# Performance work log

Measured on AMD Instinct MI355X. Metric: run time of the kernel, lower is better.

## Reference

```python
import jax, jax.numpy as jnp
import numpy as np

B, T, D, H, DH, F, E, TOPK = 4, 1024, 1024, 16, 64, 4096, 8, 2
GATE_TEMP = 0.9
EPS = 1e-5


def _ln(x, g, b):
    m = jnp.mean(x, axis=-1, keepdims=True)
    v = jnp.mean((x - m) ** 2, axis=-1, keepdims=True)
    return (x - m) * jax.lax.rsqrt(v + EPS) * g + b


def setup_inputs() -> dict:
    key = jax.random.key(0)
    ks = jax.random.split(key, 16)
    s = 0.02
    inp = {
        'x': jax.random.normal(ks[0], (B, T, D), jnp.float32),
        'mask': jnp.tril(jnp.ones((1, 1, T, T), jnp.int32)),  # causal
        'ln1_g': jnp.ones((D,), jnp.float32), 'ln1_b': jnp.zeros((D,), jnp.float32),
        'wq': jax.random.normal(ks[1], (D, D), jnp.float32) * s, 'bq': jnp.zeros((D,), jnp.float32),
        'wk': jax.random.normal(ks[2], (D, D), jnp.float32) * s, 'bk': jnp.zeros((D,), jnp.float32),
        'wv': jax.random.normal(ks[3], (D, D), jnp.float32) * s, 'bv': jnp.zeros((D,), jnp.float32),
        'wo': jax.random.normal(ks[4], (D, D), jnp.float32) * s, 'bo': jnp.zeros((D,), jnp.float32),
        'ln2_g': jnp.ones((D,), jnp.float32), 'ln2_b': jnp.zeros((D,), jnp.float32),
        'gate_w': jax.random.normal(ks[5], (D, E), jnp.float32) * s, 'gate_b': jnp.zeros((E,), jnp.float32),
        'we1': jax.random.normal(ks[6], (E, D, F), jnp.float32) * s, 'be1': jnp.zeros((E, F), jnp.float32),
        'we2': jax.random.normal(ks[7], (E, F, D), jnp.float32) * s, 'be2': jnp.zeros((E, D), jnp.float32),
        'pn_g': jnp.ones((D,), jnp.float32), 'pn_b': jnp.zeros((D,), jnp.float32),
    }
    return inp


def reference(x, mask, ln1_g, ln1_b, wq, bq, wk, bk, wv, bv, wo, bo,
              ln2_g, ln2_b, gate_w, gate_b, we1, be1, we2, be2, pn_g, pn_b):
    # ---- attention branch (dropout = identity in eval) ----
    h = _ln(x, ln1_g, ln1_b)
    q = (h @ wq + bq).reshape(B, T, H, DH).transpose(0, 2, 1, 3)  # [B,H,T,DH]
    k = (h @ wk + bk).reshape(B, T, H, DH).transpose(0, 2, 1, 3)
    v = (h @ wv + bv).reshape(B, T, H, DH).transpose(0, 2, 1, 3)
    att = jnp.einsum('bhtd,bhsd->bhts', q, k) / jnp.sqrt(jnp.float32(DH))
    att = jnp.where(mask == 0, jnp.float32(-1e9), att)
    att = jax.nn.softmax(att, axis=-1)
    out = jnp.einsum('bhts,bhsd->bhtd', att, v).transpose(0, 2, 1, 3).reshape(B, T, D)
    x = x + (out @ wo + bo)

    # ---- MoE branch ----
    h = _ln(x, ln2_g, ln2_b)
    gate_logits = (h @ gate_w + gate_b) / GATE_TEMP        # [B,T,E]
    topk_vals, topk_idx = jax.lax.top_k(gate_logits, TOPK)
    keep = jnp.sum(jax.nn.one_hot(topk_idx, E, dtype=bool), axis=-2)  # [B,T,E] bool
    masked = jnp.where(keep, gate_logits, -jnp.inf)
    gate_probs = jax.nn.softmax(masked, axis=-1)            # [B,T,E]
    # dense all-expert FFN (exact GELU, dropout=identity)
    hid = jax.nn.gelu(jnp.einsum('btd,edf->btef', h, we1) + be1, approximate=False)
    expert_out = jnp.einsum('btef,efd->bted', hid, we2) + be2  # [B,T,E,D]
    moe = jnp.sum(gate_probs[..., None] * expert_out, axis=2)
    moe = _ln(moe, pn_g, pn_b)
    return x + moe
```

## Files before the change

### kernel.cpp

```cpp
#include <hip/hip_runtime.h>
#include <hip/hip_bf16.h>
#include <math.h>

#define B_ 4
#define T_ 1024
#define D_ 1024
#define H_ 16
#define DH_ 64
#define F_ 4096
#define E_ 8
#define NTOK 4096
#define EPS_ 1e-5f

typedef float f32x4 __attribute__((ext_vector_type(4)));
typedef __bf16 bf16x8 __attribute__((ext_vector_type(8)));
typedef _Float16 f16x8 __attribute__((ext_vector_type(8)));

__device__ __forceinline__ unsigned short f2bf(float f) {
    unsigned u = __float_as_uint(f);
    u = u + 0x7fffu + ((u >> 16) & 1u);
    return (unsigned short)(u >> 16);
}

__device__ __forceinline__ void splitf(float x, unsigned short& h, unsigned short& l) {
    _Float16 hf = (_Float16)x;
    _Float16 lf = (_Float16)((x - (float)hf) * 2048.0f);
    h = __builtin_bit_cast(unsigned short, hf);
    l = __builtin_bit_cast(unsigned short, lf);
}

__device__ __forceinline__ float erf_fast(float x) {
    float ax = fabsf(x);
    float t = 1.0f / fmaf(0.3275911f, ax, 1.0f);
    float y = t * fmaf(t, fmaf(t, fmaf(t, fmaf(t, 1.061405429f, -1.453152027f),
                  1.421413741f), -0.284496736f), 0.254829592f);
    float r = 1.0f - y * __expf(-ax * ax);
    return copysignf(r, x);
}

__device__ __forceinline__ void gload16(const unsigned short* g, unsigned short* l) {
    __builtin_amdgcn_global_load_lds(
        (const __attribute__((address_space(1))) unsigned int*)g,
        (__attribute__((address_space(3))) unsigned int*)l,
        16, 0, 0);
}

__device__ __forceinline__ void blockreduce2(float& s, float& sq) {
    #pragma unroll
    for (int o = 32; o > 0; o >>= 1) { s += __shfl_xor(s, o); sq += __shfl_xor(sq, o); }
    __shared__ float ls[4], lq[4];
    int w = threadIdx.x >> 6;
    if ((threadIdx.x & 63) == 0) { ls[w] = s; lq[w] = sq; }
    __syncthreads();
    s = ls[0] + ls[1] + ls[2] + ls[3];
    sq = lq[0] + lq[1] + lq[2] + lq[3];
}

__global__ void k_zero(int* __restrict__ cnt) {
    if (threadIdx.x < E_) cnt[threadIdx.x] = 0;
}

__global__ void k_tconv(const float* __restrict__ in, unsigned short* __restrict__ out,
                        int R, int C) {
    __shared__ float tile[32][33];
    int e = blockIdx.z;
    const float* ine = in + (size_t)e * R * C;
    unsigned short* oute = out + (size_t)e * R * C;
    int tx = threadIdx.x & 31, ty = threadIdx.x >> 5;
    int c0 = blockIdx.x * 32, r0 = blockIdx.y * 32;
    #pragma unroll
    for (int j = 0; j < 32; j += 8)
        tile[ty + j][tx] = ine[(size_t)(r0 + ty + j) * C + c0 + tx];
    __syncthreads();
    #pragma unroll
    for (int j = 0; j < 32; j += 8)
        oute[(size_t)(c0 + ty + j) * R + r0 + tx] = f2bf(tile[tx][ty + j]);
}

__global__ void k_tconv_split(const float* __restrict__ w0, const float* __restrict__ w1,
        const float* __restrict__ w2, const float* __restrict__ w3,
        unsigned short* __restrict__ ohi, unsigned short* __restrict__ olo) {
    __shared__ float tile[32][33];
    int z = blockIdx.z;
    const float* in = (z == 0) ? w0 : ((z == 1) ? w1 : ((z == 2) ? w2 : w3));
    unsigned short* oh = ohi + (size_t)z * D_ * D_;
    unsigned short* ol = olo + (size_t)z * D_ * D_;
    int tx = threadIdx.x & 31, ty = threadIdx.x >> 5;
    int c0 = blockIdx.x * 32, r0 = blockIdx.y * 32;
    #pragma unroll
    for (int j = 0; j < 32; j += 8)
        tile[ty + j][tx] = in[(size_t)(r0 + ty + j) * D_ + c0 + tx];
    __syncthreads();
    #pragma unroll
    for (int j = 0; j < 32; j += 8) {
        unsigned short h, l;
        splitf(tile[tx][ty + j], h, l);
        size_t o = (size_t)(c0 + ty + j) * D_ + r0 + tx;
        oh[o] = h; ol[o] = l;
    }
}

__global__ void k_ln1(const float* __restrict__ x, const float* __restrict__ g,
                      const float* __restrict__ b, unsigned short* __restrict__ hh,
                      unsigned short* __restrict__ hl) {
    int row = blockIdx.x, t = threadIdx.x;
    f32x4 v = *(const f32x4*)(x + (size_t)row * D_ + t * 4);
    float s = v.x + v.y + v.z + v.w;
    float sq = v.x * v.x + v.y * v.y + v.z * v.z + v.w * v.w;
    blockreduce2(s, sq);
    float mean = s * (1.0f / D_);
    float var = sq * (1.0f / D_) - mean * mean;
    float inv = rsqrtf(var + EPS_);
    f32x4 gv = *(const f32x4*)(g + t * 4);
    f32x4 bv = *(const f32x4*)(b + t * 4);
    ushort4 oh, ol;
    float o0 = (v.x - mean) * inv * gv.x + bv.x;
    float o1 = (v.y - mean) * inv * gv.y + bv.y;
    float o2 = (v.z - mean) * inv * gv.z + bv.z;
    float o3 = (v.w - mean) * inv * gv.w + bv.w;
    splitf(o0, oh.x, ol.x); splitf(o1, oh.y, ol.y);
    splitf(o2, oh.z, ol.z); splitf(o3, oh.w, ol.w);
    *(ushort4*)(hh + (size_t)row * D_ + t * 4) = oh;
    *(ushort4*)(hl + (size_t)row * D_ + t * 4) = ol;
}

#define LDK2 40
__device__ __forceinline__ void mfma_split(const unsigned short* __restrict__ Ah,
        const unsigned short* __restrict__ Al, int strideA, int m0,
        const unsigned short* __restrict__ Bh, const unsigned short* __restrict__ Bl,
        int strideB, int n0, int K, f32x4 acc1[4][4], f32x4 acc2[4][4]) {
    __shared__ unsigned short AsH[128 * LDK2];
    __shared__ unsigned short AsL[128 * LDK2];
    __shared__ unsigned short BsH[128 * LDK2];
    __shared__ unsigned short BsL[128 * LDK2];
    int t = threadIdx.x;
    int lane = t & 63, w = t >> 6;
    int wm = (w >> 1) * 64, wn = (w & 1) * 64;
    int r = t >> 1, kc = (t & 1) * 16;
    const unsigned short* pAh = Ah + (size_t)(m0 + r) * strideA + kc;
    const unsigned short* pAl = Al + (size_t)(m0 + r) * strideA + kc;
    const unsigned short* pBh = Bh + (size_t)(n0 + r) * strideB + kc;
    const unsigned short* pBl = Bl + (size_t)(n0 + r) * strideB + kc;
    int c15 = lane & 15, fk = (lane >> 4) * 8;
    unsigned short* wAh = &AsH[r * LDK2 + kc];
    unsigned short* wAl = &AsL[r * LDK2 + kc];
    unsigned short* wBh = &BsH[r * LDK2 + kc];
    unsigned short* wBl = &BsL[r * LDK2 + kc];
    uint4 ah0 = *(const uint4*)(pAh);
    uint4 ah1 = *(const uint4*)(pAh + 8);
    uint4 al0 = *(const uint4*)(pAl);
    uint4 al1 = *(const uint4*)(pAl + 8);
    uint4 bh0 = *(const uint4*)(pBh);
    uint4 bh1 = *(const uint4*)(pBh + 8);
    uint4 bl0 = *(const uint4*)(pBl);
    uint4 bl1 = *(const uint4*)(pBl + 8);
    for (int k0 = 0; k0 < K; k0 += 32) {
        __syncthreads();
        *(uint4*)(wAh) = ah0; *(uint4*)(wAh + 8) = ah1;
        *(uint4*)(wAl) = al0; *(uint4*)(wAl + 8) = al1;
        *(uint4*)(wBh) = bh0; *(uint4*)(wBh + 8) = bh1;
        *(uint4*)(wBl) = bl0; *(uint4*)(wBl + 8) = bl1;
        __syncthreads();
        if (k0 + 32 < K) {
            ah0 = *(const uint4*)(pAh + k0 + 32);
            ah1 = *(const uint4*)(pAh + k0 + 40);
            al0 = *(const uint4*)(pAl + k0 + 32);
            al1 = *(const uint4*)(pAl + k0 + 40);
            bh0 = *(const uint4*)(pBh + k0 + 32);
            bh1 = *(const uint4*)(pBh + k0 + 40);
            bl0 = *(const uint4*)(pBl + k0 + 32);
            bl1 = *(const uint4*)(pBl + k0 + 40);
        }
        f16x8 bfh[4], bfl[4];
        #pragma unroll
        for (int i = 0; i < 4; i++) {
            bfh[i] = *(const f16x8*)(&BsH[(wn + c15 + i * 16) * LDK2 + fk]);
            bfl[i] = *(const f16x8*)(&BsL[(wn + c15 + i * 16) * LDK2 + fk]);
        }
        #pragma unroll
        for (int mi = 0; mi < 4; mi++) {
            f16x8 afh = *(const f16x8*)(&AsH[(wm + c15 + mi * 16) * LDK2 + fk]);
            f16x8 afl = *(const f16x8*)(&AsL[(wm + c15 + mi * 16) * LDK2 + fk]);
            #pragma unroll
            for (int ni = 0; ni < 4; ni++) {
                acc1[mi][ni] = __builtin_amdgcn_mfma_f32_16x16x32_f16(afh, bfh[ni], acc1[mi][ni], 0, 0, 0);
                acc2[mi][ni] = __builtin_amdgcn_mfma_f32_16x16x32_f16(afh, bfl[ni], acc2[mi][ni], 0, 0, 0);
                acc2[mi][ni] = __builtin_amdgcn_mfma_f32_16x16x32_f16(afl, bfh[ni], acc2[mi][ni], 0, 0, 0);
            }
        }
    }
}

__global__ __launch_bounds__(256, 2) void k_qkv_split(
        const unsigned short* __restrict__ h1h, const unsigned short* __restrict__ h1l,
        const unsigned short* __restrict__ wth, const unsigned short* __restrict__ wtl,
        const float* __restrict__ bq, const float* __restrict__ bk, const float* __restrict__ bv,
        unsigned short* __restrict__ Qh, unsigned short* __restrict__ Ql,
        unsigned short* __restrict__ Kh, unsigned short* __restrict__ Kl,
        unsigned short* __restrict__ Vh, unsigned short* __restrict__ Vl) {
    int which = blockIdx.z;
    const unsigned short* Bh = wth + (size_t)which * D_ * D_;
    const unsigned short* Bl = wtl + (size_t)which * D_ * D_;
    const float* bias = (which == 0) ? bq : ((which == 1) ? bk : bv);
    unsigned short* Oh = (which == 0) ? Qh : ((which == 1) ? Kh : Vh);
    unsigned short* Ol = (which == 0) ? Ql : ((which == 1) ? Kl : Vl);
    f32x4 a1[4][4], a2[4][4];
    #pragma unroll
    for (int i = 0; i < 4; i++)
        #pragma unroll
        for (int j = 0; j < 4; j++) {
            a1[i][j].x = 0.f; a1[i][j].y = 0.f; a1[i][j].z = 0.f; a1[i][j].w = 0.f;
            a2[i][j].x = 0.f; a2[i][j].y = 0.f; a2[i][j].z = 0.f; a2[i][j].w = 0.f;
        }
    int m0 = blockIdx.y * 128, n0 = blockIdx.x * 128;
    mfma_split(h1h, h1l, D_, m0, Bh, Bl, D_, n0, D_, a1, a2);
    int lane = threadIdx.x & 63, w = threadIdx.x >> 6;
    int wm = (w >> 1) * 64, wn = (w & 1) * 64;
    int c15 = lane & 15, quad = lane >> 4;
    #pragma unroll
    for (int mi = 0; mi < 4; mi++) {
        #pragma unroll
        for (int rr = 0; rr < 4; rr++) {
            int row = m0 + wm + mi * 16 + quad * 4 + rr;
            int bidx = row >> 10, tt = row & 1023;
            #pragma unroll
            for (int ni = 0; ni < 4; ni++) {
                int col = n0 + wn + ni * 16 + c15;
                float vv = a1[mi][ni][rr] + a2[mi][ni][rr] * (1.0f / 2048.0f) + bias[col];
                unsigned short hs, ls;
                splitf(vv, hs, ls);
                size_t idx = (((size_t)bidx * H_ + (col >> 6)) * T_ + tt) * DH_ + (col & 63);
                Oh[idx] = hs; Ol[idx] = ls;
            }
        }
    }
}

__global__ __launch_bounds__(256, 2) void k_proj_split(
        const unsigned short* __restrict__ ah, const unsigned short* __restrict__ al,
        const unsigned short* __restrict__ wh, const unsigned short* __restrict__ wl,
        float* __restrict__ xp) {
    int ks = blockIdx.z;
    f32x4 a1[4][4], a2[4][4];
    #pragma unroll
    for (int i = 0; i < 4; i++)
        #pragma unroll
        for (int j = 0; j < 4; j++) {
            a1[i][j].x = 0.f; a1[i][j].y = 0.f; a1[i][j].z = 0.f; a1[i][j].w = 0.f;
            a2[i][j].x = 0.f; a2[i][j].y = 0.f; a2[i][j].z = 0.f; a2[i][j].w = 0.f;
        }
    int m0 = blockIdx.y * 128, n0 = blockIdx.x * 128;
    mfma_split(ah + ks * 512, al + ks * 512, D_, m0,
               wh + ks * 512, wl + ks * 512, D_, n0, 512, a1, a2);
    float* dst = xp + (size_t)ks * NTOK * D_;
    int lane = threadIdx.x & 63, w = threadIdx.x >> 6;
    int wm = (w >> 1) * 64, wn = (w & 1) * 64;
    int c15 = lane & 15, quad = lane >> 4;
    #pragma unroll
    for (int mi = 0; mi < 4; mi++) {
        #pragma unroll
        for (int rr = 0; rr < 4; rr++) {
            int row = m0 + wm + mi * 16 + quad * 4 + rr;
            #pragma unroll
            for (int ni = 0; ni < 4; ni++) {
                int col = n0 + wn + ni * 16 + c15;
                dst[(size_t)row * D_ + col] = a1[mi][ni][rr] + a2[mi][ni][rr] * (1.0f / 2048.0f);
            }
        }
    }
}

#define NSLOT 40
__device__ __forceinline__ int slot_base(int qt) {
    const int base[16] = {0,1,2,3,4,6,8,10,12,15,18,21,24,28,32,36};
    return base[qt];
}
__device__ __forceinline__ int swzb(int r, int cb) {
    return r * 128 + (cb ^ ((r & 7) << 4));
}
__global__ __launch_bounds__(256, 2) void k_attn1(
        const unsigned short* __restrict__ Qh, const unsigned short* __restrict__ Ql,
        const unsigned short* __restrict__ Kh, const unsigned short* __restrict__ Kl,
        const unsigned short* __restrict__ Vh, const unsigned short* __restrict__ Vl,
        float* __restrict__ opart, float* __restrict__ mlpart) {
    __shared__ unsigned short QsH[64 * 64], QsL[64 * 64];
    __shared__ unsigned short KsH[64 * 64], KsL[64 * 64];
    __shared__ unsigned short VtH[64 * 64], VtL[64 * 64];
    __shared__ unsigned short PsH[64 * 64], PsL[64 * 64];
    int sp = blockIdx.x, qt = blockIdx.y, bh = blockIdx.z;
    int lim = (qt + 1) * 64;
    int s0 = sp * 256;
    if (s0 >= lim) return;
    int ntile = min(4, (lim - s0) >> 6);
    int t = threadIdx.x;
    int lane = t & 63, w = t >> 6;
    int c15 = lane & 15, quad = lane >> 4;
    size_t bho = (size_t)bh * T_ * DH_;
    {
        int q = t >> 2, cb = (t & 3) * 32;
        const unsigned short* sh = Qh + bho + (size_t)(qt * 64 + q) * DH_ + (cb >> 1);
        const unsigned short* sl = Ql + bho + (size_t)(qt * 64 + q) * DH_ + (cb >> 1);
        uint4 h0 = *(const uint4*)(sh);
        uint4 h1 = *(const uint4*)(sh + 8);
        uint4 l0 = *(const uint4*)(sl);
        uint4 l1 = *(const uint4*)(sl + 8);
        *(uint4*)((char*)QsH + swzb(q, cb))      = h0;
        *(uint4*)((char*)QsH + swzb(q, cb + 16)) = h1;
        *(uint4*)((char*)QsL + swzb(q, cb))      = l0;
        *(uint4*)((char*)QsL + swzb(q, cb + 16)) = l1;
    }
    f32x4 o1[4], o2[4];
    #pragma unroll
    for (int i = 0; i < 4; i++) {
        o1[i].x = 0.f; o1[i].y = 0.f; o1[i].z = 0.f; o1[i].w = 0.f;
        o2[i].x = 0.f; o2[i].y = 0.f; o2[i].z = 0.f; o2[i].w = 0.f;
    }
    float m[4] = {-1e30f, -1e30f, -1e30f, -1e30f};
    float l[4] = {0.f, 0.f, 0.f, 0.f};
    int qglob0 = qt * 64 + w * 16 + quad * 4;
    for (int kt = 0; kt < ntile; kt++) {
        int kbase = s0 + kt * 64;
        __syncthreads();
        {
            int r = t >> 2, cb = (t & 3) * 32;
            const unsigned short* sh = Kh + bho + (size_t)(kbase + r) * DH_ + (cb >> 1);
            const unsigned short* sl = Kl + bho + (size_t)(kbase + r) * DH_ + (cb >> 1);
            uint4 h0 = *(const uint4*)(sh);
            uint4 h1 = *(const uint4*)(sh + 8);
            uint4 l0 = *(const uint4*)(sl);
            uint4 l1 = *(const uint4*)(sl + 8);
            *(uint4*)((char*)KsH + swzb(r, cb))      = h0;
            *(uint4*)((char*)KsH + swzb(r, cb + 16)) = h1;
            *(uint4*)((char*)KsL + swzb(r, cb))      = l0;
            *(uint4*)((char*)KsL + swzb(r, cb + 16)) = l1;
        }
        {
            int k = t & 63, d0 = (t >> 6) * 16;
            const unsigned short* vh = Vh + bho + (size_t)(kbase + k) * DH_ + d0;
            const unsigned short* vl = Vl + bho + (size_t)(kbase + k) * DH_ + d0;
            unsigned short hv[16], lv[16];
            *(uint4*)(hv) = *(const uint4*)(vh);
            *(uint4*)(hv + 8) = *(const uint4*)(vh + 8);
            *(uint4*)(lv) = *(const uint4*)(vl);
            *(uint4*)(lv + 8) = *(const uint4*)(vl + 8);
            #pragma unroll
            for (int i = 0; i < 16; i++) {
                int d = d0 + i;
                *(unsigned short*)((char*)VtH + swzb(d, k * 2)) = hv[i];
                *(unsigned short*)((char*)VtL + swzb(d, k * 2)) = lv[i];
            }
        }
        __syncthreads();
        f32x4 s1[4], s2[4];
        #pragma unroll
        for (int i = 0; i < 4; i++) {
            s1[i].x = 0.f; s1[i].y = 0.f; s1[i].z = 0.f; s1[i].w = 0.f;
            s2[i].x = 0.f; s2[i].y = 0.f; s2[i].z = 0.f; s2[i].w = 0.f;
        }
        #pragma unroll
        for (int kk = 0; kk < 2; kk++) {
            int cb = kk * 64 + quad * 16;
            f16x8 ah = *(const f16x8*)((char*)QsH + swzb(w * 16 + c15, cb));
            f16x8 al = *(const f16x8*)((char*)QsL + swzb(w * 16 + c15, cb));
            #pragma unroll
            for (int ni = 0; ni < 4; ni++) {
                f16x8 bh16 = *(const f16x8*)((char*)KsH + swzb(ni * 16 + c15, cb));
                f16x8 bl16 = *(const f16x8*)((char*)KsL + swzb(ni * 16 + c15, cb));
                s1[ni] = __builtin_amdgcn_mfma_f32_16x16x32_f16(ah, bh16, s1[ni], 0, 0, 0);
                s2[ni] = __builtin_amdgcn_mfma_f32_16x16x32_f16(ah, bl16, s2[ni], 0, 0, 0);
                s2[ni] = __builtin_amdgcn_mfma_f32_16x16x32_f16(al, bh16, s2[ni], 0, 0, 0);
            }
        }
        f32x4 p[4];
        #pragma unroll
        for (int ni = 0; ni < 4; ni++)
            p[ni] = s1[ni] * 0.125f + s2[ni] * 6.103515625e-5f;
        #pragma unroll
        for (int ni = 0; ni < 4; ni++) {
            int kglob = kbase + c15 + 16 * ni;
            #pragma unroll
            for (int r = 0; r < 4; r++)
                p[ni][r] = (kglob <= qglob0 + r) ? p[ni][r] : -1e30f;
        }
        float alpha[4];
        #pragma unroll
        for (int r = 0; r < 4; r++) {
            float rm = fmaxf(fmaxf(p[0][r], p[1][r]), fmaxf(p[2][r], p[3][r]));
            rm = fmaxf(rm, __shfl_xor(rm, 1));
            rm = fmaxf(rm, __shfl_xor(rm, 2));
            rm = fmaxf(rm, __shfl_xor(rm, 4));
            rm = fmaxf(rm, __shfl_xor(rm, 8));
            float mnew = fmaxf(m[r], rm);
            alpha[r] = __expf(m[r] - mnew);
            m[r] = mnew;
            float rs = 0.f;
            #pragma unroll
            for (int ni = 0; ni < 4; ni++) {
                float pv = (p[ni][r] > -1e29f) ? __expf(p[ni][r] - mnew) : 0.f;
                p[ni][r] = pv;
                rs += pv;
            }
            rs += __shfl_xor(rs, 1);
            rs += __shfl_xor(rs, 2);
            rs += __shfl_xor(rs, 4);
            rs += __shfl_xor(rs, 8);
            l[r] = l[r] * alpha[r] + rs;
        }
        #pragma unroll
        for (int ni = 0; ni < 4; ni++) {
            o1[ni].x *= alpha[0]; o1[ni].y *= alpha[1]; o1[ni].z *= alpha[2]; o1[ni].w *= alpha[3];
            o2[ni].x *= alpha[0]; o2[ni].y *= alpha[1]; o2[ni].z *= alpha[2]; o2[ni].w *= alpha[3];
        }
        #pragma unroll
        for (int ni = 0; ni < 4; ni++) {
            int cbyte = (c15 + 16 * ni) * 2;
            #pragma unroll
            for (int r = 0; r < 4; r++) {
                unsigned short hs, ls;
                splitf(p[ni][r], hs, ls);
                int row = w * 16 + quad * 4 + r;
                *(unsigned short*)((char*)PsH + swzb(row, cbyte)) = hs;
                *(unsigned short*)((char*)PsL + swzb(row, cbyte)) = ls;
            }
        }
        __syncthreads();
        #pragma unroll
        for (int kk = 0; kk < 2; kk++) {
            int cb = kk * 64 + quad * 16;
            f16x8 ph = *(const f16x8*)((char*)PsH + swzb(w * 16 + c15, cb));
            f16x8 pl = *(const f16x8*)((char*)PsL + swzb(w * 16 + c15, cb));
            #pragma unroll
            for (int ni = 0; ni < 4; ni++) {
                f16x8 vh16 = *(const f16x8*)((char*)VtH + swzb(ni * 16 + c15, cb));
                f16x8 vl16 = *(const f16x8*)((char*)VtL + swzb(ni * 16 + c15, cb));
                o1[ni] = __builtin_amdgcn_mfma_f32_16x16x32_f16(ph, vh16, o1[ni], 0, 0, 0);
                o2[ni] = __builtin_amdgcn_mfma_f32_16x16x32_f16(ph, vl16, o2[ni], 0, 0, 0);
                o2[ni] = __builtin_amdgcn_mfma_f32_16x16x32_f16(pl, vh16, o2[ni], 0, 0, 0);
            }
        }
    }
    int slot = bh * NSLOT + slot_base(qt) + sp;
    float* dst = opart + (size_t)slot * 64 * 64;
    #pragma unroll
    for (int ni = 0; ni < 4; ni++) {
        #pragma unroll
        for (int r = 0; r < 4; r++) {
            float val = o1[ni][r] + o2[ni][r] * (1.0f / 2048.0f);
            dst[(size_t)(w * 16 + quad * 4 + r) * 64 + c15 + 16 * ni] = val;
        }
    }
    if (c15 == 0) {
        #pragma unroll
        for (int r = 0; r < 4; r++) {
            int row = w * 16 + quad * 4 + r;
            mlpart[slot * 128 + row * 2 + 0] = m[r];
            mlpart[slot * 128 + row * 2 + 1] = l[r];
        }
    }
}

__global__ void k_attn2(const float* __restrict__ opart, const float* __restrict__ mlpart,
                        unsigned short* __restrict__ atth, unsigned short* __restrict__ attl) {
    int qt = blockIdx.x, bh = blockIdx.y;
    int b = bh >> 4, h = bh & 15;
    int nsp = (qt >> 2) + 1;
    int slot0 = bh * NSLOT + slot_base(qt);
    int tid = threadIdx.x;
    int q = tid >> 2, d0 = (tid & 3) * 16;
    float ms[4], ls[4];
    float mx = -1e30f;
    for (int s = 0; s < nsp; s++) {
        ms[s] = mlpart[(slot0 + s) * 128 + q * 2 + 0];
        ls[s] = mlpart[(slot0 + s) * 128 + q * 2 + 1];
        mx = fmaxf(mx, ms[s]);
    }
    float den = 0.f;
    f32x4 num[4];
    #pragma unroll
    for (int i = 0; i < 4; i++) { num[i].x = 0.f; num[i].y = 0.f; num[i].z = 0.f; num[i].w = 0.f; }
    for (int s = 0; s < nsp; s++) {
        float sc = __expf(ms[s] - mx);
        den += ls[s] * sc;
        const float* src = opart + ((size_t)(slot0 + s) * 64 + q) * 64 + d0;
        #pragma unroll
        for (int i = 0; i < 4; i++) num[i] += sc * *(const f32x4*)(src + i * 4);
    }
    float inv = 1.0f / den;
    size_t base = ((size_t)(b * T_ + qt * 64 + q)) * D_ + h * DH_ + d0;
    #pragma unroll
    for (int i = 0; i < 4; i++) {
        f32x4 v = num[i] * inv;
        ushort4 hh, ll;
        splitf(v.x, hh.x, ll.x); splitf(v.y, hh.y, ll.y);
        splitf(v.z, hh.z, ll.z); splitf(v.w, hh.w, ll.w);
        *(ushort4*)(atth + base + i * 4) = hh;
        *(ushort4*)(attl + base + i * 4) = ll;
    }
}

__global__ void k_ln2_gate(const float* __restrict__ xp, const float* __restrict__ bo,
        const float* __restrict__ xin, float* __restrict__ x2,
        const float* __restrict__ g, const float* __restrict__ bb,
        const float* __restrict__ gw, const float* __restrict__ gb,
        unsigned short* __restrict__ h2, int* __restrict__ cnt, int* __restrict__ lst,
        int* __restrict__ te, int* __restrict__ ts, float* __restrict__ tp) {
    int row = blockIdx.x, t = threadIdx.x;
    f32x4 v = *(const f32x4*)(xp + (size_t)row * D_ + t * 4)
            + *(const f32x4*)(xp + (size_t)NTOK * D_ + (size_t)row * D_ + t * 4)
            + *(const f32x4*)(bo + t * 4)
            + *(const f32x4*)(xin + (size_t)row * D_ + t * 4);
    *(f32x4*)(x2 + (size_t)row * D_ + t * 4) = v;
    float s = v.x + v.y + v.z + v.w;
    float sq = v.x * v.x + v.y * v.y + v.z * v.z + v.w * v.w;
    blockreduce2(s, sq);
    float mean = s * (1.0f / D_), var = sq * (1.0f / D_) - mean * mean;
    float inv = rsqrtf(var + EPS_);
    f32x4 gv = *(const f32x4*)(g + t * 4);
    f32x4 bv = *(const f32x4*)(bb + t * 4);
    float hv[4];
    #pragma unroll
    for (int i = 0; i < 4; i++) hv[i] = (v[i] - mean) * inv * gv[i] + bv[i];
    ushort4 hb;
    hb.x = f2bf(hv[0]); hb.y = f2bf(hv[1]); hb.z = f2bf(hv[2]); hb.w = f2bf(hv[3]);
    *(ushort4*)(&h2[(size_t)row * D_ + t * 4]) = hb;
    float lg[8];
    #pragma unroll
    for (int e2 = 0; e2 < 8; e2++) lg[e2] = 0.f;
    #pragma unroll
    for (int i = 0; i < 4; i++) {
        const float* gr = gw + (size_t)(t * 4 + i) * E_;
        f32x4 g0 = *(const f32x4*)(gr);
        f32x4 g1 = *(const f32x4*)(gr + 4);
        lg[0] = fmaf(hv[i], g0.x, lg[0]); lg[1] = fmaf(hv[i], g0.y, lg[1]);
        lg[2] = fmaf(hv[i], g0.z, lg[2]); lg[3] = fmaf(hv[i], g0.w, lg[3]);
        lg[4] = fmaf(hv[i], g1.x, lg[4]); lg[5] = fmaf(hv[i], g1.y, lg[5]);
        lg[6] = fmaf(hv[i], g1.z, lg[6]); lg[7] = fmaf(hv[i], g1.w, lg[7]);
    }
    #pragma unroll
    for (int o = 32; o > 0; o >>= 1) {
        #pragma unroll
        for (int e2 = 0; e2 < 8; e2++) lg[e2] += __shfl_xor(lg[e2], o);
    }
    __shared__ float lred[4][8];
    int w = t >> 6;
    if ((t & 63) == 0) {
        #pragma unroll
        for (int e2 = 0; e2 < 8; e2++) lred[w][e2] = lg[e2];
    }
    __syncthreads();
    if (t == 0) {
        float L[8];
        #pragma unroll
        for (int e2 = 0; e2 < 8; e2++)
            L[e2] = (lred[0][e2] + lred[1][e2] + lred[2][e2] + lred[3][e2] + gb[e2]) / 0.9f;
        int e0 = 0, e1 = -1; float v0 = L[0], v1 = -3e38f;
        #pragma unroll
        for (int e2 = 1; e2 < 8; e2++) {
            float xv = L[e2];
            if (xv > v0)      { v1 = v0; e1 = e0; v0 = xv; e0 = e2; }
            else if (xv > v1) { v1 = xv; e1 = e2; }
        }
        float ex = __expf(v1 - v0);
        float denom = 1.0f + ex;
        float p0 = 1.0f / denom, p1 = ex / denom;
        int s0 = atomicAdd(&cnt[e0], 1);
        int s1 = atomicAdd(&cnt[e1], 1);
        lst[e0 * NTOK + s0] = row;
        lst[e1 * NTOK + s1] = row;
        te[row * 2 + 0] = e0; te[row * 2 + 1] = e1;
        ts[row * 2 + 0] = s0; ts[row * 2 + 1] = s1;
        tp[row * 2 + 0] = p0; tp[row * 2 + 1] = p1;
    }
}

__global__ void k_offs(const int* __restrict__ cnt, int* __restrict__ offs) {
    if (threadIdx.x == 0 && blockIdx.x == 0) {
        int a = 0;
        #pragma unroll
        for (int e = 0; e < E_; e++) { offs[e] = a; a += cnt[e]; }
    }
}

__device__ __forceinline__ void mfma_core(const unsigned short* __restrict__ A, int strideA,
        const int* __restrict__ gather, int m0, int M,
        const unsigned short* __restrict__ Bt, int strideB, int n0, int K, f32x4 acc[4][4]) {
    __shared__ unsigned short As[128 * 32];
    __shared__ unsigned short Bs[128 * 32];
    int t = threadIdx.x;
    int lane = t & 63, wid = t >> 6;
    int wm = (wid >> 1) * 64, wn = (wid & 1) * 64;
    int c15 = lane & 15, fk = (lane >> 4) * 8;
    int r0 = wid * 32 + (lane >> 2);
    int kc2 = (lane & 3) * 8;
    int ar0, ar1;
    {
        int mm0 = m0 + r0, mm1 = m0 + r0 + 16;
        if (gather) { ar0 = gather[mm0 < M ? mm0 : 0]; ar1 = gather[mm1 < M ? mm1 : 0]; }
        else        { ar0 = mm0; ar1 = mm1; }
    }
    const unsigned short* pA0 = A + (size_t)ar0 * strideA + kc2;
    const unsigned short* pA1 = A + (size_t)ar1 * strideA + kc2;
    const unsigned short* pB0 = Bt + (size_t)(n0 + r0) * strideB + kc2;
    const unsigned short* pB1 = Bt + (size_t)(n0 + r0 + 16) * strideB + kc2;
    unsigned short* lA0 = As + (wid * 2 + 0) * 512;
    unsigned short* lA1 = As + (wid * 2 + 1) * 512;
    unsigned short* lB0 = Bs + (wid * 2 + 0) * 512;
    unsigned short* lB1 = Bs + (wid * 2 + 1) * 512;
    for (int k0 = 0; k0 < K; k0 += 32) {
        __syncthreads();
        gload16(pA0 + k0, lA0);
        gload16(pA1 + k0, lA1);
        gload16(pB0 + k0, lB0);
        gload16(pB1 + k0, lB1);
        __syncthreads();
        bf16x8 af[4], bfr[4];
        #pragma unroll
        for (int i = 0; i < 4; i++) {
            af[i]  = *(const bf16x8*)(&As[(wm + c15 + i * 16) * 32 + fk]);
            bfr[i] = *(const bf16x8*)(&Bs[(wn + c15 + i * 16) * 32 + fk]);
        }
        #pragma unroll
        for (int mi = 0; mi < 4; mi++)
            #pragma unroll
            for (int ni = 0; ni < 4; ni++)
                acc[mi][ni] = __builtin_amdgcn_mfma_f32_16x16x32_bf16(af[mi], bfr[ni], acc[mi][ni], 0, 0, 0);
    }
}

__global__ __launch_bounds__(256, 2) void k_moe1(const unsigned short* __restrict__ h2,
        const unsigned short* __restrict__ w1t, const float* __restrict__ be1,
        const int* __restrict__ cnt, const int* __restrict__ offs, const int* __restrict__ lst,
        unsigned short* __restrict__ hid) {
    int flat = blockIdx.x + (blockIdx.y << 5) + (blockIdx.z << 10);
    int sfl = ((flat & 7) << 10) + (flat >> 3);
    int bx = sfl & 31, by = (sfl >> 5) & 31, e = sfl >> 10;
    int M = cnt[e];
    int m0 = by * 128;
    if (m0 >= M) return;
    int n0 = bx * 128;
    f32x4 acc[4][4];
    #pragma unroll
    for (int i = 0; i < 4; i++)
        #pragma unroll
        for (int j = 0; j < 4; j++) { acc[i][j].x = 0.f; acc[i][j].y = 0.f; acc[i][j].z = 0.f; acc[i][j].w = 0.f; }
    mfma_core(h2, D_, lst + e * NTOK, m0, M, w1t + (size_t)e * F_ * D_, D_, n0, D_, acc);
    int lane = threadIdx.x & 63, w = threadIdx.x >> 6;
    int wm = (w >> 1) * 64, wn = (w & 1) * 64;
    int base = offs[e];
    const float* b1 = be1 + (size_t)e * F_;
    int c15 = lane & 15, quad = lane >> 4;
    #pragma unroll
    for (int mi = 0; mi < 4; mi++) {
        #pragma unroll
        for (int rr = 0; rr < 4; rr++) {
            int row = m0 + wm + mi * 16 + quad * 4 + rr;
            if (row < M) {
                size_t rb = (size_t)(base + row) * F_;
                #pragma unroll
                for (int ni = 0; ni < 4; ni++) {
                    int col = n0 + wn + ni * 16 + c15;
                    float xv = acc[mi][ni][rr] + b1[col];
                    float ge = 0.5f * xv * (1.0f + erf_fast(xv * 0.70710678118654752f));
                    hid[rb + col] = f2bf(ge);
                }
            }
        }
    }
}

__global__ __launch_bounds__(256, 2) void k_moe2(const unsigned short* __restrict__ hid,
        const unsigned short* __restrict__ w2t,
        const int* __restrict__ cnt, const int* __restrict__ offs, float* __restrict__ eop) {
    int flat = blockIdx.x + (blockIdx.y << 3) + (blockIdx.z << 8);
    int sfl = ((flat & 7) << 9) + (flat >> 3);
    int bx = sfl & 7, by = (sfl >> 3) & 31, ez = sfl >> 8;
    int e = ez >> 1, ks = ez & 1;
    int M = cnt[e];
    int m0 = by * 128;
    if (m0 >= M) return;
    int n0 = bx * 128;
    int base = offs[e];
    f32x4 acc[4][4];
    #pragma unroll
    for (int i = 0; i < 4; i++)
        #pragma unroll
        for (int j = 0; j < 4; j++) { acc[i][j].x = 0.f; acc[i][j].y = 0.f; acc[i][j].z = 0.f; acc[i][j].w = 0.f; }
    mfma_core(hid + (size_t)base * F_ + ks * (F_ / 2), F_, nullptr, m0, M,
              w2t + (size_t)e * D_ * F_ + ks * (F_ / 2), F_, n0, F_ / 2, acc);
    float* dst = eop + (size_t)ks * 2 * NTOK * D_ + (size_t)base * D_;
    int lane = threadIdx.x & 63, w = threadIdx.x >> 6;
    int wm = (w >> 1) * 64, wn = (w & 1) * 64;
    int c15 = lane & 15, quad = lane >> 4;
    #pragma unroll
    for (int mi = 0; mi < 4; mi++) {
        #pragma unroll
        for (int rr = 0; rr < 4; rr++) {
            int row = m0 + wm + mi * 16 + quad * 4 + rr;
            if (row < M) {
                #pragma unroll
                for (int ni = 0; ni < 4; ni++) {
                    int col = n0 + wn + ni * 16 + c15;
                    dst[(size_t)row * D_ + col] = acc[mi][ni][rr];
                }
            }
        }
    }
}

__global__ void k_final(const float* __restrict__ x2, const float* __restrict__ eop,
        const float* __restrict__ be2,
        const int* __restrict__ te, const int* __restrict__ ts, const float* __restrict__ tp,
        const int* __restrict__ offs, const float* __restrict__ png, const float* __restrict__ pnb,
        float* __restrict__ out) {
    int row = blockIdx.x, t = threadIdx.x;
    int e0 = te[row * 2], e1 = te[row * 2 + 1];
    size_t g0 = (size_t)(offs[e0] + ts[row * 2]);
    size_t g1 = (size_t)(offs[e1] + ts[row * 2 + 1]);
    float p0 = tp[row * 2], p1 = tp[row * 2 + 1];
    const size_t HALF = (size_t)2 * NTOK * D_;
    f32x4 a = *(const f32x4*)(eop + g0 * D_ + t * 4)
            + *(const f32x4*)(eop + HALF + g0 * D_ + t * 4)
            + *(const f32x4*)(be2 + (size_t)e0 * D_ + t * 4);
    f32x4 b = *(const f32x4*)(eop + g1 * D_ + t * 4)
            + *(const f32x4*)(eop + HALF + g1 * D_ + t * 4)
            + *(const f32x4*)(be2 + (size_t)e1 * D_ + t * 4);
    f32x4 mo = p0 * a + p1 * b;
    float s = mo.x + mo.y + mo.z + mo.w;
    float sq = mo.x * mo.x + mo.y * mo.y + mo.z * mo.z + mo.w * mo.w;
    blockreduce2(s, sq);
    float mean = s * (1.0f / D_), var = sq * (1.0f / D_) - mean * mean;
    float inv = rsqrtf(var + EPS_);
    f32x4 gv = *(const f32x4*)(png + t * 4);
    f32x4 bv = *(const f32x4*)(pnb + t * 4);
    f32x4 xv = *(const f32x4*)(x2 + (size_t)row * D_ + t * 4);
    f32x4 o;
    o.x = xv.x + (mo.x - mean) * inv * gv.x + bv.x;
    o.y = xv.y + (mo.y - mean) * inv * gv.y + bv.y;
    o.z = xv.z + (mo.z - mean) * inv * gv.z + bv.z;
    o.w = xv.w + (mo.w - mean) * inv * gv.w + bv.w;
    *(f32x4*)(out + (size_t)row * D_ + t * 4) = o;
}

extern "C" void kernel_launch(void* const* d_in, const int* in_sizes, int n_in,
                              void* d_out, int out_size, void* d_ws, size_t ws_size,
                              hipStream_t stream) {
    (void)in_sizes; (void)n_in; (void)out_size; (void)ws_size;
    const float* x    = (const float*)d_in[0];
    const float* ln1g = (const float*)d_in[2];
    const float* ln1b = (const float*)d_in[3];
    const float* wq   = (const float*)d_in[4];
    const float* bq   = (const float*)d_in[5];
    const float* wk   = (const float*)d_in[6];
    const float* bk   = (const float*)d_in[7];
    const float* wv   = (const float*)d_in[8];
    const float* bv   = (const float*)d_in[9];
    const float* wo   = (const float*)d_in[10];
    const float* bo   = (const float*)d_in[11];
    const float* ln2g = (const float*)d_in[12];
    const float* ln2b = (const float*)d_in[13];
    const float* gw   = (const float*)d_in[14];
    const float* gb   = (const float*)d_in[15];
    const float* we1  = (const float*)d_in[16];
    const float* be1  = (const float*)d_in[17];
    const float* we2  = (const float*)d_in[18];
    const float* be2  = (const float*)d_in[19];
    const float* png  = (const float*)d_in[20];
    const float* pnb  = (const float*)d_in[21];
    float* out = (float*)d_out;

    char* ws = (char*)d_ws;
    size_t off = 0;
    auto alloc = [&](size_t bytes) { void* p = ws + off; off += (bytes + 255) & ~(size_t)255; return p; };
    unsigned short* h1h = (unsigned short*)alloc((size_t)NTOK * D_ * 2);
    unsigned short* h1l = (unsigned short*)alloc((size_t)NTOK * D_ * 2);
    unsigned short* Qhp = (unsigned short*)alloc((size_t)NTOK * D_ * 2);
    unsigned short* Qlp = (unsigned short*)alloc((size_t)NTOK * D_ * 2);
    unsigned short* Khp = (unsigned short*)alloc((size_t)NTOK * D_ * 2);
    unsigned short* Klp = (unsigned short*)alloc((size_t)NTOK * D_ * 2);
    unsigned short* Vhp = (unsigned short*)alloc((size_t)NTOK * D_ * 2);
    unsigned short* Vlp = (unsigned short*)alloc((size_t)NTOK * D_ * 2);
    unsigned short* atth = (unsigned short*)alloc((size_t)NTOK * D_ * 2);
    unsigned short* attl = (unsigned short*)alloc((size_t)NTOK * D_ * 2);
    float* x2  = (float*)alloc((size_t)NTOK * D_ * 4);
    unsigned short* h2  = (unsigned short*)alloc((size_t)NTOK * D_ * 2);
    unsigned short* w1t = (unsigned short*)alloc((size_t)E_ * D_ * F_ * 2);
    unsigned short* w2t = (unsigned short*)alloc((size_t)E_ * D_ * F_ * 2);
    unsigned short* hid = (unsigned short*)alloc((size_t)(2 * NTOK + 128) * F_ * 2);
    float* opart = (float*)alloc((size_t)64 * NSLOT * 64 * 64 * 4);
    float* mlpart= (float*)alloc((size_t)64 * NSLOT * 128 * 4);
    unsigned short* wsh = (unsigned short*)alloc((size_t)4 * D_ * D_ * 2);
    unsigned short* wsl = (unsigned short*)alloc((size_t)4 * D_ * D_ * 2);
    int* cnt   = (int*)alloc(256);
    int* offs  = (int*)alloc(256);
    int* lst   = (int*)alloc((size_t)E_ * NTOK * 4);
    int* te    = (int*)alloc((size_t)NTOK * 2 * 4);
    int* ts    = (int*)alloc((size_t)NTOK * 2 * 4);
    float* tp  = (float*)alloc((size_t)NTOK * 2 * 4);
    float* xp  = opart;
    float* eop = (float*)h1h;

    k_zero<<<dim3(1), dim3(64), 0, stream>>>(cnt);
    k_tconv<<<dim3(F_ / 32, D_ / 32, E_), dim3(256), 0, stream>>>(we1, w1t, D_, F_);
    k_tconv<<<dim3(D_ / 32, F_ / 32, E_), dim3(256), 0, stream>>>(we2, w2t, F_, D_);
    k_tconv_split<<<dim3(D_ / 32, D_ / 32, 4), dim3(256), 0, stream>>>(wq, wk, wv, wo, wsh, wsl);
    k_ln1<<<dim3(NTOK), dim3(256), 0, stream>>>(x, ln1g, ln1b, h1h, h1l);
    k_qkv_split<<<dim3(D_ / 128, NTOK / 128, 3), dim3(256), 0, stream>>>(
        h1h, h1l, wsh, wsl, bq, bk, bv, Qhp, Qlp, Khp, Klp, Vhp, Vlp);
    k_attn1<<<dim3(4, T_ / 64, B_ * H_), dim3(256), 0, stream>>>(
        Qhp, Qlp, Khp, Klp, Vhp, Vlp, opart, mlpart);
    k_attn2<<<dim3(T_ / 64, B_ * H_), dim3(256), 0, stream>>>(opart, mlpart, atth, attl);
    k_proj_split<<<dim3(D_ / 128, NTOK / 128, 2), dim3(256), 0, stream>>>(
        atth, attl, wsh + (size_t)3 * D_ * D_, wsl + (size_t)3 * D_ * D_, xp);
    k_ln2_gate<<<dim3(NTOK), dim3(256), 0, stream>>>(
        xp, bo, x, x2, ln2g, ln2b, gw, gb, h2, cnt, lst, te, ts, tp);
    k_offs<<<dim3(1), dim3(64), 0, stream>>>(cnt, offs);
    k_moe1<<<dim3(F_ / 128, NTOK / 128, E_), dim3(256), 0, stream>>>(h2, w1t, be1, cnt, offs, lst, hid);
    k_moe2<<<dim3(D_ / 128, NTOK / 128, E_ * 2), dim3(256), 0, stream>>>(hid, w2t, cnt, offs, eop);
    k_final<<<dim3(NTOK), dim3(256), 0, stream>>>(x2, eop, be2, te, ts, tp, offs, png, pnb, out);
}
```

Before: 968.1 us.

## Prefetch K/V into registers, keep Q in registers, swizzle GEMM LDS layout

The attention kernel now holds the Q fragments in registers instead of staging them through shared memory. It also prefetches the next K/V tile into registers while the current tile is being computed. The V transpose now writes packed 32-bit pairs, and the occupancy hint is raised to 3 blocks. Separately, the shared GEMM core XOR-swizzles its LDS column chunks on both store and read to cut bank conflicts. The trade-off is more register pressure in attention, which may conflict with the higher occupancy target.

```diff
diff --git a/kernel.cpp b/kernel.cpp
--- a/kernel.cpp
+++ b/kernel.cpp
@@ -278,12 +278,11 @@
 __device__ __forceinline__ int swzb(int r, int cb) {
     return r * 128 + (cb ^ ((r & 7) << 4));
 }
-__global__ __launch_bounds__(256, 2) void k_attn1(
+__global__ __launch_bounds__(256, 3) void k_attn1(
         const unsigned short* __restrict__ Qh, const unsigned short* __restrict__ Ql,
         const unsigned short* __restrict__ Kh, const unsigned short* __restrict__ Kl,
         const unsigned short* __restrict__ Vh, const unsigned short* __restrict__ Vl,
         float* __restrict__ opart, float* __restrict__ mlpart) {
-    __shared__ unsigned short QsH[64 * 64], QsL[64 * 64];
     __shared__ unsigned short KsH[64 * 64], KsL[64 * 64];
     __shared__ unsigned short VtH[64 * 64], VtL[64 * 64];
     __shared__ unsigned short PsH[64 * 64], PsL[64 * 64];
@@ -296,19 +295,29 @@
     int lane = t & 63, w = t >> 6;
     int c15 = lane & 15, quad = lane >> 4;
     size_t bho = (size_t)bh * T_ * DH_;
+    f16x8 qfh[2], qfl[2];
     {
-        int q = t >> 2, cb = (t & 3) * 32;
-        const unsigned short* sh = Qh + bho + (size_t)(qt * 64 + q) * DH_ + (cb >> 1);
-        const unsigned short* sl = Ql + bho + (size_t)(qt * 64 + q) * DH_ + (cb >> 1);
-        uint4 h0 = *(const uint4*)(sh);
-        uint4 h1 = *(const uint4*)(sh + 8);
-        uint4 l0 = *(const uint4*)(sl);
-        uint4 l1 = *(const uint4*)(sl + 8);
-        *(uint4*)((char*)QsH + swzb(q, cb))      = h0;
-        *(uint4*)((char*)QsH + swzb(q, cb + 16)) = h1;
-        *(uint4*)((char*)QsL + swzb(q, cb))      = l0;
-        *(uint4*)((char*)QsL + swzb(q, cb + 16)) = l1;
-    }
+        const unsigned short* qb = Qh + bho + (size_t)(qt * 64 + w * 16 + c15) * DH_ + quad * 8;
+        const unsigned short* ql2 = Ql + bho + (size_t)(qt * 64 + w * 16 + c15) * DH_ + quad * 8;
+        qfh[0] = *(const f16x8*)(qb);
+        qfh[1] = *(const f16x8*)(qb + 32);
+        qfl[0] = *(const f16x8*)(ql2);
+        qfl[1] = *(const f16x8*)(ql2 + 32);
+    }
+    int kr = t >> 2, kcb = (t & 3) * 32;
+    int vkp = (t & 31) * 2, vd0 = (t >> 5) * 8;
+    uint4 kh0, kh1, kl0, kl1, vh0, vh1, vl0, vl1;
+    auto loadKV = [&](int kbase) {
+        const unsigned short* sh = Kh + bho + (size_t)(kbase + kr) * DH_ + (kcb >> 1);
+        const unsigned short* sl = Kl + bho + (size_t)(kbase + kr) * DH_ + (kcb >> 1);
+        kh0 = *(const uint4*)(sh);     kh1 = *(const uint4*)(sh + 8);
+        kl0 = *(const uint4*)(sl);     kl1 = *(const uint4*)(sl + 8);
+        const unsigned short* vh = Vh + bho + (size_t)(kbase + vkp) * DH_ + vd0;
+        const unsigned short* vl = Vl + bho + (size_t)(kbase + vkp) * DH_ + vd0;
+        vh0 = *(const uint4*)(vh);     vh1 = *(const uint4*)(vh + DH_);
+        vl0 = *(const uint4*)(vl);     vl1 = *(const uint4*)(vl + DH_);
+    };
+    loadKV(s0);
     f32x4 o1[4], o2[4];
     #pragma unroll
     for (int i = 0; i < 4; i++) {
@@ -321,36 +330,25 @@
     for (int kt = 0; kt < ntile; kt++) {
         int kbase = s0 + kt * 64;
         __syncthreads();
+        *(uint4*)((char*)KsH + swzb(kr, kcb))      = kh0;
+        *(uint4*)((char*)KsH + swzb(kr, kcb + 16)) = kh1;
+        *(uint4*)((char*)KsL + swzb(kr, kcb))      = kl0;
+        *(uint4*)((char*)KsL + swzb(kr, kcb + 16)) = kl1;
         {
-            int r = t >> 2, cb = (t & 3) * 32;
-            const unsigned short* sh = Kh + bho + (size_t)(kbase + r) * DH_ + (cb >> 1);
-            const unsigned short* sl = Kl + bho + (size_t)(kbase + r) * DH_ + (cb >> 1);
-            uint4 h0 = *(const uint4*)(sh);
-            uint4 h1 = *(const uint4*)(sh + 8);
-            uint4 l0 = *(const uint4*)(sl);
-            uint4 l1 = *(const uint4*)(sl + 8);
-            *(uint4*)((char*)KsH + swzb(r, cb))      = h0;
-            *(uint4*)((char*)KsH + swzb(r, cb + 16)) = h1;
-            *(uint4*)((char*)KsL + swzb(r, cb))      = l0;
-            *(uint4*)((char*)KsL + swzb(r, cb + 16)) = l1;
-        }
-        {
-            int k = t & 63, d0 = (t >> 6) * 16;
-            const unsigned short* vh = Vh + bho + (size_t)(kbase + k) * DH_ + d0;
-            const unsigned short* vl = Vl + bho + (size_t)(kbase + k) * DH_ + d0;
-            unsigned short hv[16], lv[16];
-            *(uint4*)(hv) = *(const uint4*)(vh);
-            *(uint4*)(hv + 8) = *(const uint4*)(vh + 8);
-            *(uint4*)(lv) = *(const uint4*)(vl);
-            *(uint4*)(lv + 8) = *(const uint4*)(vl + 8);
-            #pragma unroll
-            for (int i = 0; i < 16; i++) {
-                int d = d0 + i;
-                *(unsigned short*)((char*)VtH + swzb(d, k * 2)) = hv[i];
-                *(unsigned short*)((char*)VtL + swzb(d, k * 2)) = lv[i];
+            unsigned short h0a[8], h1a[8], l0a[8], l1a[8];
+            *(uint4*)h0a = vh0; *(uint4*)h1a = vh1;
+            *(uint4*)l0a = vl0; *(uint4*)l1a = vl1;
+            #pragma unroll
+            for (int i = 0; i < 8; i++) {
+                int d = vd0 + i;
+                unsigned hv32 = (unsigned)h0a[i] | ((unsigned)h1a[i] << 16);
+                unsigned lv32 = (unsigned)l0a[i] | ((unsigned)l1a[i] << 16);
+                *(unsigned*)((char*)VtH + swzb(d, vkp * 2)) = hv32;
+                *(unsigned*)((char*)VtL + swzb(d, vkp * 2)) = lv32;
             }
         }
         __syncthreads();
+        if (kt + 1 < ntile) loadKV(kbase + 64);
         f32x4 s1[4], s2[4];
         #pragma unroll
         for (int i = 0; i < 4; i++) {
@@ -360,8 +358,8 @@
         #pragma unroll
         for (int kk = 0; kk < 2; kk++) {
             int cb = kk * 64 + quad * 16;
-            f16x8 ah = *(const f16x8*)((char*)QsH + swzb(w * 16 + c15, cb));
-            f16x8 al = *(const f16x8*)((char*)QsL + swzb(w * 16 + c15, cb));
+            f16x8 ah = qfh[kk];
+            f16x8 al = qfl[kk];
             #pragma unroll
             for (int ni = 0; ni < 4; ni++) {
                 f16x8 bh16 = *(const f16x8*)((char*)KsH + swzb(ni * 16 + c15, cb));
@@ -589,9 +587,10 @@
     int t = threadIdx.x;
     int lane = t & 63, wid = t >> 6;
     int wm = (wid >> 1) * 64, wn = (wid & 1) * 64;
-    int c15 = lane & 15, fk = (lane >> 4) * 8;
+    int c15 = lane & 15;
+    int fk = (((lane >> 4) ^ ((c15 >> 1) & 3)) * 8);
     int r0 = wid * 32 + (lane >> 2);
-    int kc2 = (lane & 3) * 8;
+    int kc2 = (((lane & 3) ^ ((lane >> 3) & 3)) * 8);
     int ar0, ar1;
     {
         int mm0 = m0 + r0, mm1 = m0 + r0 + 16;
```

Measured after the change: 985.1 us. No clear change (+1.8%).
